# Kernel tuning notes

Measured on AMD Instinct MI355X. Metric: run time of the kernel, lower is better.

The kernel has to match this reference:

```python
import jax, jax.numpy as jnp
import numpy as np
import math

B, N, D, L, H, FF, T = 8, 256, 384, 6, 8, 1536, 4
Dh = D // H  # 48, divisible by 6 for 3D rotary
N_M1 = T + 1 + 2 * N  # learn tokens + state + hand + head
S = 2 * N_M1


def rotary_pe_3d(x, coords):
    # x: [B,H,S,Dh], coords: [B,S,3]. Split head dim into 3 axis chunks,
    # apply standard RoPE per axis using the continuous coordinate as position.
    dh = x.shape[-1]
    d = dh // 3
    half = d // 2
    inv_freq = 1.0 / (10000.0 ** (jnp.arange(half, dtype=x.dtype) / half))
    outs = []
    for a in range(3):
        xa = x[..., a * d:(a + 1) * d]
        ang = coords[..., a][:, None, :, None] * inv_freq  # [B,1,S,half]
        c, s = jnp.cos(ang), jnp.sin(ang)
        x1, x2 = xa[..., :half], xa[..., half:]
        outs.append(jnp.concatenate([x1 * c - x2 * s, x1 * s + x2 * c], axis=-1))
    return jnp.concatenate(outs, axis=-1)


def layernorm(x, g, b):
    m = jnp.mean(x, axis=-1, keepdims=True)
    v = jnp.var(x, axis=-1, keepdims=True)
    return (x - m) * jax.lax.rsqrt(v + 1e-5) * g + b


def transformer_layer(src, coords_src, mask, Wq, bq, Wk, bk, Wv, bv, Wo, bo, W1, b1, W2, b2, g1, be1, g2, be2):
    Bsz, Ss, _ = src.shape
    q = jnp.einsum('bsd,od->bso', src, Wq) + bq
    k = jnp.einsum('bsd,od->bso', src, Wk) + bk
    v = jnp.einsum('bsd,od->bso', src, Wv) + bv
    q = q.reshape(Bsz, Ss, H, Dh).transpose(0, 2, 1, 3)
    k = k.reshape(Bsz, Ss, H, Dh).transpose(0, 2, 1, 3)
    v = v.reshape(Bsz, Ss, H, Dh).transpose(0, 2, 1, 3)
    q = rotary_pe_3d(q, coords_src)
    k = rotary_pe_3d(k, coords_src)
    scores = jnp.einsum('bhqd,bhkd->bhqk', q, k) / math.sqrt(Dh)
    scores = jnp.where(mask[None, None, :, :], -jnp.inf, scores)
    attn = jnp.einsum('bhqk,bhkd->bhqd', jax.nn.softmax(scores, axis=-1), v)
    attn = attn.transpose(0, 2, 1, 3).reshape(Bsz, Ss, D)
    attn = jnp.einsum('bsd,od->bso', attn, Wo) + bo
    src2 = layernorm(src + attn, g1, be1)
    ff = jnp.einsum('bsf,of->bso', jax.nn.gelu(jnp.einsum('bsd,fd->bsf', src2, W1) + b1, approximate=False), W2) + b2
    return layernorm(src2 + ff, g2, be2)


def setup_inputs() -> dict:
    key = jax.random.key(0)
    ks = jax.random.split(key, 32)
    rnd = lambda i, shape, scale=1.0: (jax.random.normal(ks[i], shape, dtype=jnp.float32) * scale)
    inp = {
        'hand_token_t': rnd(0, (B, N, D)),
        'head_token_t': rnd(1, (B, N, D)),
        'hand_token_m1': rnd(2, (B, N, D)),
        'head_token_m1': rnd(3, (B, N, D)),
        'coords_hand_t': rnd(4, (B, N, 3)),
        'coords_head_t': rnd(5, (B, N, 3)),
        'coords_hand_m1': rnd(6, (B, N, 3)),
        'coords_head_m1': rnd(7, (B, N, 3)),
        'state_t': rnd(8, (B, D)),
        'state_m1': rnd(9, (B, D)),
        'trans_head_t': rnd(10, (B, 3)),
        'trans_head_m1': rnd(11, (B, 3)),
        'tokens_m1': rnd(12, (1, T, D), 0.02),
        'tokens_t': rnd(13, (1, T, D), 0.02),
        'Wq': rnd(14, (L, D, D), 0.02), 'bq': jnp.zeros((L, D), jnp.float32),
        'Wk': rnd(15, (L, D, D), 0.02), 'bk': jnp.zeros((L, D), jnp.float32),
        'Wv': rnd(16, (L, D, D), 0.02), 'bv': jnp.zeros((L, D), jnp.float32),
        'Wo': rnd(17, (L, D, D), 0.02), 'bo': jnp.zeros((L, D), jnp.float32),
        'W1': rnd(18, (L, FF, D), 0.02), 'b1': jnp.zeros((L, FF), jnp.float32),
        'W2': rnd(19, (L, D, FF), 0.02), 'b2': jnp.zeros((L, D), jnp.float32),
        'g1': jnp.ones((L, D), jnp.float32), 'be1': jnp.zeros((L, D), jnp.float32),
        'g2': jnp.ones((L, D), jnp.float32), 'be2': jnp.zeros((L, D), jnp.float32),
    }
    return inp


def reference(hand_token_t, head_token_t, hand_token_m1, head_token_m1,
              coords_hand_t, coords_head_t, coords_hand_m1, coords_head_m1,
              state_t, state_m1, trans_head_t, trans_head_m1,
              tokens_m1, tokens_t, Wq, bq, Wk, bk, Wv, bv, Wo, bo,
              W1, b1, W2, b2, g1, be1, g2, be2):
    # Build token sequence: [state_m1, hand_m1, head_m1, learn_m1, state_t, hand_t, head_t, learn_t]
    tok_m1 = jnp.broadcast_to(tokens_m1, (B, T, D))
    tok_t = jnp.broadcast_to(tokens_t, (B, T, D))
    coord_m1 = jnp.broadcast_to(trans_head_m1[:, None, :], (B, T, 3))
    coord_t = jnp.broadcast_to(trans_head_t[:, None, :], (B, T, 3))
    src = jnp.concatenate([
        state_m1[:, None, :], hand_token_m1, head_token_m1, tok_m1,
        state_t[:, None, :], hand_token_t, head_token_t, tok_t], axis=1)
    coords_src = jnp.concatenate([
        trans_head_m1[:, None, :], coords_hand_m1, coords_head_m1, coord_m1,
        trans_head_t[:, None, :], coords_hand_t, coords_head_t, coord_t], axis=1)
    # block-causal mask: m1 block cannot attend to t block
    mask = jnp.zeros((S, S), dtype=bool).at[:N_M1, N_M1:].set(True)
    for i in range(L):
        src = transformer_layer(src, coords_src, mask,
                                Wq[i], bq[i], Wk[i], bk[i], Wv[i], bv[i], Wo[i], bo[i],
                                W1[i], b1[i], W2[i], b2[i], g1[i], be1[i], g2[i], be2[i])
    return src[:, -T:, :]
```

## Files before the change

kernel.cpp:

```cpp
#include <hip/hip_runtime.h>
#include <hip/hip_bf16.h>
#include <math.h>

#define BB 8
#define NN 256
#define DD 384
#define LL 6
#define HH 8
#define FFD 1536
#define TT 4
#define DH 48
#define NM1 517
#define SS 1034
#define SSP 1088
#define MROWS (BB*SS)
#define NQKV 1152
#define QSCALE2 (0.14433756729740643f * 1.4426950408889634f)

typedef unsigned short u16;
typedef unsigned int u32;
typedef short bf8 __attribute__((ext_vector_type(8)));
typedef float f32x4 __attribute__((ext_vector_type(4)));

__device__ __forceinline__ u16 f2bf(float f) {
  __hip_bfloat16 h = __float2bfloat16(f);
  return *reinterpret_cast<u16*>(&h);
}
__device__ __forceinline__ float bf2f(u16 u) {
  __hip_bfloat16 h;
  *reinterpret_cast<u16*>(&h) = u;
  return __bfloat162float(h);
}
__device__ __forceinline__ float max3f(float a, float b, float c) {
  return fmaxf(fmaxf(a, b), c);
}
__device__ __forceinline__ void async16(void* lds, const void* g) {
  __builtin_amdgcn_global_load_lds(
      (const __attribute__((address_space(1))) unsigned int*)g,
      (__attribute__((address_space(3))) unsigned int*)lds, 16, 0, 0);
}

__global__ void build_src(const float* __restrict__ hand_t, const float* __restrict__ head_t,
                          const float* __restrict__ hand_m1, const float* __restrict__ head_m1,
                          const float* __restrict__ state_t, const float* __restrict__ state_m1,
                          const float* __restrict__ tok_m1, const float* __restrict__ tok_t,
                          float* __restrict__ src, u16* __restrict__ srcb) {
  int idx = blockIdx.x * 256 + threadIdx.x;
  if (idx >= BB * SS * DD) return;
  int d = idx % DD;
  int bs = idx / DD;
  int s = bs % SS;
  int b = bs / SS;
  float val;
  if (s == 0)               val = state_m1[b * DD + d];
  else if (s <= NN)         val = hand_m1[((size_t)(b * NN + (s - 1))) * DD + d];
  else if (s <= 2 * NN)     val = head_m1[((size_t)(b * NN + (s - 1 - NN))) * DD + d];
  else if (s <= 2 * NN + TT) val = tok_m1[(s - (2 * NN + 1)) * DD + d];
  else if (s == NM1)        val = state_t[b * DD + d];
  else if (s <= NM1 + NN)   val = hand_t[((size_t)(b * NN + (s - NM1 - 1))) * DD + d];
  else if (s <= NM1 + 2 * NN) val = head_t[((size_t)(b * NN + (s - NM1 - 1 - NN))) * DD + d];
  else                      val = tok_t[(s - (NM1 + 2 * NN + 1)) * DD + d];
  src[idx] = val;
  srcb[idx] = f2bf(val);
}

__global__ void build_coords(const float* __restrict__ c_hand_t, const float* __restrict__ c_head_t,
                             const float* __restrict__ c_hand_m1, const float* __restrict__ c_head_m1,
                             const float* __restrict__ tr_t, const float* __restrict__ tr_m1,
                             float* __restrict__ coords) {
  int idx = blockIdx.x * 256 + threadIdx.x;
  if (idx >= BB * SS * 3) return;
  int a = idx % 3;
  int bs = idx / 3;
  int s = bs % SS;
  int b = bs / SS;
  float val;
  if (s == 0)               val = tr_m1[b * 3 + a];
  else if (s <= NN)         val = c_hand_m1[(b * NN + (s - 1)) * 3 + a];
  else if (s <= 2 * NN)     val = c_head_m1[(b * NN + (s - 1 - NN)) * 3 + a];
  else if (s <= 2 * NN + TT) val = tr_m1[b * 3 + a];
  else if (s == NM1)        val = tr_t[b * 3 + a];
  else if (s <= NM1 + NN)   val = c_hand_t[(b * NN + (s - NM1 - 1)) * 3 + a];
  else if (s <= NM1 + 2 * NN) val = c_head_t[(b * NN + (s - NM1 - 1 - NN)) * 3 + a];
  else                      val = tr_t[b * 3 + a];
  coords[idx] = val;
}

__global__ void build_trig(const float* __restrict__ coords, float2* __restrict__ trig) {
  int idx = blockIdx.x * 256 + threadIdx.x;
  if (idx >= BB * SS * 24) return;
  int i = idx & 7;
  int axis = (idx >> 3) % 3;
  int bs = idx / 24;
  float cv = coords[bs * 3 + axis];
  float inv = expf(-(float)i * 1.1512925464970229f);
  float ang = cv * inv;
  trig[idx] = make_float2(cosf(ang), sinf(ang));
}

__global__ void cvt_bf(const float* __restrict__ in, u16* __restrict__ out, int n4) {
  int idx = blockIdx.x * 256 + threadIdx.x;
  if (idx >= n4) return;
  float4 v = reinterpret_cast<const float4*>(in)[idx];
  short4 o;
  o.x = (short)f2bf(v.x); o.y = (short)f2bf(v.y);
  o.z = (short)f2bf(v.z); o.w = (short)f2bf(v.w);
  reinterpret_cast<short4*>(out)[idx] = o;
}

__global__ void pack_qkv(const float* __restrict__ Wq, const float* __restrict__ Wk,
                         const float* __restrict__ Wv, u16* __restrict__ wqkv) {
  int idx = blockIdx.x * 256 + threadIdx.x;
  const int TOTAL = LL * NQKV * 96;
  if (idx >= TOTAL) return;
  int k4 = idx % 96;
  int n = (idx / 96) % NQKV;
  int l = idx / (96 * NQKV);
  int sel = n / 384, nn = n - sel * 384;
  const float* W = (sel == 0) ? Wq : ((sel == 1) ? Wk : Wv);
  float4 v = *reinterpret_cast<const float4*>(W + ((size_t)l * 384 + nn) * 384 + k4 * 4);
  short4 o;
  o.x = (short)f2bf(v.x); o.y = (short)f2bf(v.y);
  o.z = (short)f2bf(v.z); o.w = (short)f2bf(v.w);
  *reinterpret_cast<short4*>(wqkv + ((size_t)(l * NQKV + n) * 384 + k4 * 4)) = o;
}

__global__ void pack_bqkv(const float* __restrict__ bq, const float* __restrict__ bk,
                          const float* __restrict__ bv, float* __restrict__ bqkv) {
  int idx = blockIdx.x * 256 + threadIdx.x;
  if (idx >= LL * NQKV) return;
  int n = idx % NQKV, l = idx / NQKV;
  int sel = n / 384, nn = n - sel * 384;
  const float* Bp = (sel == 0) ? bq : ((sel == 1) ? bk : bv);
  bqkv[idx] = Bp[l * 384 + nn];
}

__global__ void pad_vt(u16* __restrict__ vt) {
  int idx = blockIdx.x * 256 + threadIdx.x;
  const int PADW = SSP - SS;
  if (idx >= 64 * DH * PADW) return;
  int c = idx % PADW;
  int rd = idx / PADW;
  vt[(size_t)rd * SSP + SS + c] = 0;
}

__global__ void pad_qk(u16* __restrict__ qh, u16* __restrict__ kh) {
  int idx = blockIdx.x * 256 + threadIdx.x;
  if (idx >= 64 * SS * 16) return;
  int c = idx & 15;
  int row = idx >> 4;
  qh[(size_t)row * 64 + 48 + c] = 0;
  kh[(size_t)row * 64 + 48 + c] = 0;
}

template <int EPI, int OUT, int Nc, int Kc>
__global__ __launch_bounds__(512) void gemm_as(
    const u16* __restrict__ Ab, const u16* __restrict__ Wb,
    const float* __restrict__ bias, const float2* __restrict__ trig,
    const float* __restrict__ Rf,
    float* __restrict__ Cf, u16* __restrict__ Cb,
    u16* __restrict__ Ck, u16* __restrict__ Cv) {
  constexpr int BUFSZ = 24576;
  constexpr int M = MROWS;
  constexpr int nxt = Nc >> 6;
  __shared__ __align__(16) char sm[2 * BUFSZ];
  const int tid = threadIdx.x;

  const int gL = blockIdx.x;
  const int x8 = gL & 7, jj = gL >> 3;
  const int jjm = jj / nxt;
  const int cnt = (x8 == 0) ? 9 : 8;
  if (jjm >= cnt) return;
  const int mt_ = ((x8 == 0) ? 0 : 9 + (x8 - 1) * 8) + jjm;
  const int bm = mt_ << 7, bn = (jj % nxt) << 6;

  const int lid = tid & 63, w = tid >> 6;
  const int wm = w >> 1, wn = w & 1;
  const int l15 = lid & 15, lg = lid >> 4;
  const int lr = lid >> 3, lu = lid & 7;
  const int swz = lu ^ lr;
  f32x4 acc[2][2] = {};

  auto stage = [&](int bsel, int k0) {
    char* base = sm + bsel * BUFSZ;
#pragma unroll
    for (int q = 0; q < 2; ++q) {
      int row = w * 16 + q * 8 + lr;
      int grow = bm + row; if (grow >= M) grow = M - 1;
      async16(base + w * 2048 + q * 1024, Ab + (size_t)grow * Kc + k0 + (swz << 3));
    }
    async16(base + 16384 + w * 1024, Wb + (size_t)(bn + w * 8 + lr) * Kc + k0 + (swz << 3));
  };

  stage(0, 0);
  int bs = 0;

#pragma unroll
  for (int k0 = 0; k0 < Kc; k0 += 64) {
    if (k0 + 64 < Kc) {
      stage(bs ^ 1, k0 + 64);
      asm volatile("s_waitcnt vmcnt(3)" ::: "memory");
    } else {
      asm volatile("s_waitcnt vmcnt(0)" ::: "memory");
    }
    __builtin_amdgcn_s_barrier();
    const char* base = sm + bs * BUFSZ;
    bf8 a[2][2], bfr[2][2];
#pragma unroll
    for (int kf = 0; kf < 2; ++kf) {
#pragma unroll
      for (int mt = 0; mt < 2; ++mt) {
        int row = wm * 32 + mt * 16 + l15;
        int off = ((row << 7) + (kf << 6) + (lg << 4)) ^ ((row & 7) << 4);
        a[kf][mt] = *reinterpret_cast<const bf8*>(base + off);
      }
#pragma unroll
      for (int nt = 0; nt < 2; ++nt) {
        int row = wn * 32 + nt * 16 + l15;
        int off = 16384 + (((row << 7) + (kf << 6) + (lg << 4)) ^ ((row & 7) << 4));
        bfr[kf][nt] = *reinterpret_cast<const bf8*>(base + off);
      }
    }
#pragma unroll
    for (int kf = 0; kf < 2; ++kf)
#pragma unroll
      for (int mt = 0; mt < 2; ++mt)
#pragma unroll
        for (int nt = 0; nt < 2; ++nt)
          acc[mt][nt] = __builtin_amdgcn_mfma_f32_16x16x32_bf16(a[kf][mt], bfr[kf][nt], acc[mt][nt], 0, 0, 0);
    asm volatile("s_waitcnt lgkmcnt(0)" ::: "memory");
    __builtin_amdgcn_s_barrier();
    bs ^= 1;
  }

  if constexpr (OUT != 2) {
#pragma unroll
    for (int nt = 0; nt < 2; ++nt) {
      const int n = bn + wn * 32 + nt * 16 + l15;
      const float bsv = bias[n];
#pragma unroll
      for (int mt = 0; mt < 2; ++mt) {
        const int m0 = bm + wm * 32 + mt * 16 + lg * 4;
#pragma unroll
        for (int r = 0; r < 4; ++r) {
          int m = m0 + r;
          if (m >= M) continue;
          float v = acc[mt][nt][r] + bsv;
          if (EPI == 1) v = 0.5f * v * (1.0f + erff(v * 0.70710678118654752f));
          if (OUT == 0) Cf[(size_t)m * Nc + n] = v + Rf[(size_t)m * Nc + n];
          else          Cb[(size_t)m * Nc + n] = f2bf(v);
        }
      }
    }
  } else {
    float* tile = (float*)sm;
#pragma unroll
    for (int nt = 0; nt < 2; ++nt) {
      const int nl = wn * 32 + nt * 16 + l15;
      const float bsv = bias[bn + nl];
#pragma unroll
      for (int mt = 0; mt < 2; ++mt) {
#pragma unroll
        for (int r = 0; r < 4; ++r) {
          int ml = wm * 32 + mt * 16 + lg * 4 + r;
          tile[ml * 65 + nl] = acc[mt][nt][r] + bsv;
        }
      }
    }
    __syncthreads();
    const int bnm = bn % 384;
    const int sel = bn / 384;
    if (sel < 2) {
      u16* Cqk = (sel == 0) ? Cb : Ck;
      const int d = lid;
      const int nn_ = bnm + d;
      const int hdiv = nn_ / 48, hrem = nn_ - hdiv * 48;
      const int axis = hrem >> 4, ii = hrem & 7;
      const bool hi = (hrem & 8) != 0;
      for (int si = 0; si < 16; ++si) {
        int row = w * 16 + si;
        int m = bm + row;
        if (m >= M) break;
        int bI = m / SS, s = m - bI * SS;
        float v = tile[row * 65 + d];
        float p = tile[row * 65 + (d ^ 8)];
        float2 t = trig[(size_t)(bI * SS + s) * 24 + axis * 8 + ii];
        float outv = hi ? (p * t.y + v * t.x) : (v * t.x - p * t.y);
        if (sel == 0) outv *= QSCALE2;
        Cqk[((size_t)(bI * HH + hdiv) * SS + s) * 64 + hrem] = f2bf(outv);
      }
    } else {
      const int srow = tid & 127, dq = tid >> 7;
      const int m = bm + srow;
      if (m < M) {
        int bI = m / SS, s = m - bI * SS;
        for (int di = 0; di < 16; ++di) {
          int d = dq * 16 + di;
          int nn_ = bnm + d;
          int hdiv = nn_ / 48, hrem = nn_ - hdiv * 48;
          Cv[((size_t)(bI * HH + hdiv) * DH + hrem) * SSP + s] = f2bf(tile[srow * 65 + d]);
        }
      }
    }
  }
}

__global__ __launch_bounds__(512) void attn_mfma(const u16* __restrict__ qh,
                                                 const u16* __restrict__ kh,
                                                 const u16* __restrict__ vt,
                                                 u16* __restrict__ outb) {
  __shared__ __align__(16) char sm[32768];
  const int tid = threadIdx.x;
  const int lid = tid & 63, w = tid >> 6;
  const int l15 = lid & 15, lg = lid >> 4;
  const int lr = lid >> 3, lu = lid & 7;
  const int swz8 = (lu ^ lr) << 3;

  const int f = blockIdx.x;
  const int low = f & 7, j = f >> 3;
  const int gi = j / 9, qp = j - gi * 9;
  const int g = gi * 8 + low;
  const int h = g & 7, b = g >> 3;
  const int qblk = (qp < 5) ? (4 + qp) : (qp - 5);
  const int bh = b * HH + h;
  const int q0w = qblk * 128 + w * 16;
  const u16* kbase = kh + (size_t)bh * SS * 64;
  const u16* vbase = vt + (size_t)bh * DH * SSP;

  bf8 qf[2];
  {
    int row = q0w + l15; if (row >= SS) row = SS - 1;
    const u16* qp_ = qh + ((size_t)bh * SS + row) * 64;
    qf[0] = *reinterpret_cast<const bf8*>(qp_ + lg * 8);
    qf[1] = *reinterpret_cast<const bf8*>(qp_ + 32 + lg * 8);
  }
  const int qrow = q0w + l15;

  float m_q = -1e30f, l_q = 0.f;
  f32x4 accO[3] = {};

  const int nch = (qblk < 4) ? 9 : 17;

  auto stage = [&](int bsel, int c) {
    const int j0 = c * 64;
    char* kb = sm + bsel * 16384;
    char* vb = kb + 8192;
    {
      int s = w * 8 + lr;
      int jt_ = s >> 4, lgs = (s >> 2) & 3, rr = s & 3;
      int p = ((jt_ >> 1) << 5) + (lgs << 3) + ((jt_ & 1) << 2) + rr;
      int jrow = j0 + p; if (jrow >= SS) jrow = SS - 1;
      async16(kb + w * 1024, kbase + (size_t)jrow * 64 + swz8);
    }
    {
      int vrow = w * 8 + lr; if (vrow >= DH) vrow = DH - 1;
      async16(vb + w * 1024, vbase + (size_t)vrow * SSP + j0 + swz8);
    }
  };

  stage(0, 0);
  __syncthreads();
  int bsel = 0;

  for (int c = 0; c < nch; ++c) {
    if (c + 1 < nch) {
      stage(bsel ^ 1, c + 1);
      asm volatile("s_waitcnt vmcnt(2)" ::: "memory");
    } else {
      asm volatile("s_waitcnt vmcnt(0)" ::: "memory");
    }
    __builtin_amdgcn_s_barrier();
    const int j0 = c * 64;
    const char* kb = sm + bsel * 16384;
    const char* vb = kb + 8192;

    f32x4 sv[4];
    __builtin_amdgcn_s_setprio(1);
#pragma unroll
    for (int jt = 0; jt < 4; ++jt) {
      int row = jt * 16 + l15;
      int off0 = ((row << 7) + (lg << 4)) ^ ((row & 7) << 4);
      int off1 = ((row << 7) + 64 + (lg << 4)) ^ ((row & 7) << 4);
      bf8 kb0 = *reinterpret_cast<const bf8*>(kb + off0);
      bf8 kb1 = *reinterpret_cast<const bf8*>(kb + off1);
      f32x4 z = {};
      z = __builtin_amdgcn_mfma_f32_16x16x32_bf16(kb0, qf[0], z, 0, 0, 0);
      z = __builtin_amdgcn_mfma_f32_16x16x32_bf16(kb1, qf[1], z, 0, 0, 0);
      sv[jt] = z;
    }
    __builtin_amdgcn_s_setprio(0);

    const bool domask = (c == 16) | ((q0w < NM1) & (c >= 8));
    if (domask) {
#pragma unroll
      for (int jt = 0; jt < 4; ++jt)
#pragma unroll
        for (int r = 0; r < 4; ++r) {
          int kabs = j0 + ((jt >> 1) << 5) + (lg << 3) + ((jt & 1) << 2) + r;
          if (kabs >= SS || (qrow < NM1 && kabs >= NM1)) sv[jt][r] = -1e30f;
        }
    }

    float mx = max3f(sv[0][0], sv[0][1], sv[0][2]);
    mx = max3f(mx, sv[0][3], sv[1][0]);
    mx = max3f(mx, sv[1][1], sv[1][2]);
    mx = max3f(mx, sv[1][3], sv[2][0]);
    mx = max3f(mx, sv[2][1], sv[2][2]);
    mx = max3f(mx, sv[2][3], sv[3][0]);
    mx = max3f(mx, sv[3][1], sv[3][2]);
    mx = fmaxf(mx, sv[3][3]);
    mx = fmaxf(mx, __shfl_xor(mx, 16));
    mx = fmaxf(mx, __shfl_xor(mx, 32));

    const bool skip = __all(mx <= m_q);
    const float mn = skip ? m_q : fmaxf(m_q, mx);

    float pv[4][4];
    float ps = 0.f;
#pragma unroll
    for (int jt = 0; jt < 4; ++jt)
#pragma unroll
      for (int r = 0; r < 4; ++r) {
        float p = __builtin_amdgcn_exp2f(sv[jt][r] - mn);
        pv[jt][r] = p;
        ps += p;
      }
    ps += __shfl_xor(ps, 16);
    ps += __shfl_xor(ps, 32);

    if (!skip) {
      float alpha = __builtin_amdgcn_exp2f(m_q - mn);
      l_q = l_q * alpha + ps;
      m_q = mn;
      const int lg4 = lg * 4;
      float a0 = __shfl(alpha, lg4);
      float a1 = __shfl(alpha, lg4 + 1);
      float a2 = __shfl(alpha, lg4 + 2);
      float a3 = __shfl(alpha, lg4 + 3);
#pragma unroll
      for (int dt = 0; dt < 3; ++dt) {
        accO[dt][0] *= a0; accO[dt][1] *= a1;
        accO[dt][2] *= a2; accO[dt][3] *= a3;
      }
    } else {
      l_q += ps;
    }

    bf8 pa[2];
#pragma unroll
    for (int jc = 0; jc < 2; ++jc) {
      u32 w0 = (u32)f2bf(pv[jc * 2][0])     | ((u32)f2bf(pv[jc * 2][1]) << 16);
      u32 w1 = (u32)f2bf(pv[jc * 2][2])     | ((u32)f2bf(pv[jc * 2][3]) << 16);
      u32 w2 = (u32)f2bf(pv[jc * 2 + 1][0]) | ((u32)f2bf(pv[jc * 2 + 1][1]) << 16);
      u32 w3 = (u32)f2bf(pv[jc * 2 + 1][2]) | ((u32)f2bf(pv[jc * 2 + 1][3]) << 16);
      uint4 t = make_uint4(w0, w1, w2, w3);
      pa[jc] = *reinterpret_cast<bf8*>(&t);
    }

    __builtin_amdgcn_s_setprio(1);
#pragma unroll
    for (int dt = 0; dt < 3; ++dt) {
      int row = dt * 16 + l15;
#pragma unroll
      for (int jc = 0; jc < 2; ++jc) {
        int off = ((row << 7) + (jc << 6) + (lg << 4)) ^ ((row & 7) << 4);
        bf8 vb8 = *reinterpret_cast<const bf8*>(vb + off);
        accO[dt] = __builtin_amdgcn_mfma_f32_16x16x32_bf16(pa[jc], vb8, accO[dt], 0, 0, 0);
      }
    }
    __builtin_amdgcn_s_setprio(0);
    asm volatile("s_waitcnt lgkmcnt(0)" ::: "memory");
    __builtin_amdgcn_s_barrier();
    bsel ^= 1;
  }

  float linv = 1.0f / l_q;
  const int lg4 = lg * 4;
  float il[4];
#pragma unroll
  for (int r = 0; r < 4; ++r) il[r] = __shfl(linv, lg4 + r);
#pragma unroll
  for (int r = 0; r < 4; ++r) {
    int q = q0w + lg4 + r;
    if (q >= SS) continue;
#pragma unroll
    for (int dt = 0; dt < 3; ++dt) {
      int d = dt * 16 + l15;
      outb[((size_t)(b * SS + q)) * DD + h * DH + d] = f2bf(accO[dt][r] * il[r]);
    }
  }
}

__global__ __launch_bounds__(512) void add_ln(const float* __restrict__ a,
                                              const float* __restrict__ g,
                                              const float* __restrict__ be,
                                              float* __restrict__ out,
                                              u16* __restrict__ outb) {
  const int w = threadIdx.x >> 6, lane = threadIdx.x & 63;
  const int row = blockIdx.x * 8 + w;
  const size_t base = (size_t)row * DD;
  float x[6];
#pragma unroll
  for (int jj = 0; jj < 6; ++jj) x[jj] = a[base + lane + 64 * jj];
  float s = x[0] + x[1] + x[2] + x[3] + x[4] + x[5];
#pragma unroll
  for (int off = 32; off; off >>= 1) s += __shfl_xor(s, off);
  float mean = s * (1.0f / 384.0f);
  float dv[6], vs = 0.f;
#pragma unroll
  for (int jj = 0; jj < 6; ++jj) { dv[jj] = x[jj] - mean; vs += dv[jj] * dv[jj]; }
#pragma unroll
  for (int off = 32; off; off >>= 1) vs += __shfl_xor(vs, off);
  float rs = rsqrtf(vs * (1.0f / 384.0f) + 1e-5f);
#pragma unroll
  for (int jj = 0; jj < 6; ++jj) {
    int c = lane + 64 * jj;
    float o = dv[jj] * rs * g[c] + be[c];
    out[base + c] = o;
    outb[base + c] = f2bf(o);
  }
}

__global__ void copy_out(const float* __restrict__ src, float* __restrict__ out) {
  int idx = blockIdx.x * 256 + threadIdx.x;
  if (idx >= BB * TT * DD) return;
  int d = idx % DD;
  int bt = idx / DD;
  int t = bt % TT;
  int b = bt / TT;
  out[idx] = src[((size_t)b * SS + (SS - TT) + t) * DD + d];
}

extern "C" void kernel_launch(void* const* d_in, const int* in_sizes, int n_in,
                              void* d_out, int out_size, void* d_ws, size_t ws_size,
                              hipStream_t stream) {
  const float* hand_t    = (const float*)d_in[0];
  const float* head_t    = (const float*)d_in[1];
  const float* hand_m1   = (const float*)d_in[2];
  const float* head_m1   = (const float*)d_in[3];
  const float* c_hand_t  = (const float*)d_in[4];
  const float* c_head_t  = (const float*)d_in[5];
  const float* c_hand_m1 = (const float*)d_in[6];
  const float* c_head_m1 = (const float*)d_in[7];
  const float* state_t   = (const float*)d_in[8];
  const float* state_m1  = (const float*)d_in[9];
  const float* tr_t      = (const float*)d_in[10];
  const float* tr_m1     = (const float*)d_in[11];
  const float* tok_m1    = (const float*)d_in[12];
  const float* tok_t     = (const float*)d_in[13];
  const float* Wq = (const float*)d_in[14];
  const float* bq = (const float*)d_in[15];
  const float* Wk = (const float*)d_in[16];
  const float* bk = (const float*)d_in[17];
  const float* Wv = (const float*)d_in[18];
  const float* bv = (const float*)d_in[19];
  const float* Wo = (const float*)d_in[20];
  const float* bo = (const float*)d_in[21];
  const float* W1 = (const float*)d_in[22];
  const float* b1 = (const float*)d_in[23];
  const float* W2 = (const float*)d_in[24];
  const float* b2 = (const float*)d_in[25];
  const float* g1 = (const float*)d_in[26];
  const float* be1 = (const float*)d_in[27];
  const float* g2 = (const float*)d_in[28];
  const float* be2 = (const float*)d_in[29];

  const size_t SRC_N = (size_t)BB * SS * DD;
  float* src    = (float*)d_ws;
  float* src2   = src + SRC_N;
  float* bufB   = src2 + SRC_N;
  float* coords = bufB + SRC_N;
  float* bqkv   = coords + (size_t)BB * SS * 3;
  float2* trig  = (float2*)(bqkv + (size_t)LL * NQKV);
  u16* srcb  = (u16*)(trig + (size_t)BB * SS * 24);
  u16* src2b = srcb + SRC_N;
  u16* attnb = src2b + SRC_N;
  u16* qh  = attnb + SRC_N;
  const size_t QH_N = (size_t)BB * HH * SS * 64;
  u16* khb = qh + QH_N;
  u16* vtb = khb + QH_N;
  u16* hbf = vtb + (size_t)64 * DH * SSP;
  u16* wqkv_b = hbf + (size_t)MROWS * FFD;
  const size_t WD = (size_t)LL * DD * DD;
  const size_t WF = (size_t)LL * FFD * DD;
  u16* wo_bf = wqkv_b + (size_t)LL * NQKV * 384;
  u16* w1_bf = wo_bf + WD;
  u16* w2_bf = w1_bf + WF;

  dim3 blk(256);
  dim3 blk512(512);

  build_src<<<(BB * SS * DD + 255) / 256, blk, 0, stream>>>(
      hand_t, head_t, hand_m1, head_m1, state_t, state_m1, tok_m1, tok_t, src, srcb);
  build_coords<<<(BB * SS * 3 + 255) / 256, blk, 0, stream>>>(
      c_hand_t, c_head_t, c_hand_m1, c_head_m1, tr_t, tr_m1, coords);
  build_trig<<<(BB * SS * 24 + 255) / 256, blk, 0, stream>>>(coords, trig);
  pack_qkv<<<(LL * NQKV * 96 + 255) / 256, blk, 0, stream>>>(Wq, Wk, Wv, wqkv_b);
  pack_bqkv<<<(LL * NQKV + 255) / 256, blk, 0, stream>>>(bq, bk, bv, bqkv);
  cvt_bf<<<(int)(WD / 4 + 255) / 256, blk, 0, stream>>>(Wo, wo_bf, (int)(WD / 4));
  cvt_bf<<<(int)(WF / 4 + 255) / 256, blk, 0, stream>>>(W1, w1_bf, (int)(WF / 4));
  cvt_bf<<<(int)(WF / 4 + 255) / 256, blk, 0, stream>>>(W2, w2_bf, (int)(WF / 4));
  pad_vt<<<(64 * DH * (SSP - SS) + 255) / 256, blk, 0, stream>>>(vtb);
  pad_qk<<<(64 * SS * 16 + 255) / 256, blk, 0, stream>>>(qh, khb);

  dim3 gqkv(18 * 72);
  dim3 gwo(6 * 72);
  dim3 gf1(24 * 72);
  dim3 gf2(6 * 72);
  dim3 gattn(9 * 8 * 8);

  for (int l = 0; l < LL; ++l) {
    const u16* Wqkv_l = wqkv_b + (size_t)l * NQKV * 384;
    const u16* Wo_l = wo_bf + (size_t)l * DD * DD;
    const u16* W1_l = w1_bf + (size_t)l * FFD * DD;
    const u16* W2_l = w2_bf + (size_t)l * DD * FFD;

    gemm_as<0, 2, NQKV, DD><<<gqkv, blk512, 0, stream>>>(
        srcb, Wqkv_l, bqkv + l * NQKV, trig, nullptr, nullptr, qh, khb, vtb);
    attn_mfma<<<gattn, blk512, 0, stream>>>(qh, khb, vtb, attnb);
    gemm_as<0, 0, DD, DD><<<gwo, blk512, 0, stream>>>(
        attnb, Wo_l, bo + l * DD, nullptr, src, bufB, nullptr, nullptr, nullptr);
    add_ln<<<MROWS / 8, blk512, 0, stream>>>(bufB, g1 + l * DD, be1 + l * DD, src2, src2b);
    gemm_as<1, 1, FFD, DD><<<gf1, blk512, 0, stream>>>(
        src2b, W1_l, b1 + l * FFD, nullptr, nullptr, nullptr, hbf, nullptr, nullptr);
    gemm_as<0, 0, DD, FFD><<<gf2, blk512, 0, stream>>>(
        hbf, W2_l, b2 + l * DD, nullptr, src2, bufB, nullptr, nullptr, nullptr);
    add_ln<<<MROWS / 8, blk512, 0, stream>>>(bufB, g2 + l * DD, be2 + l * DD, src, srcb);
  }
  copy_out<<<(BB * TT * DD + 255) / 256, blk, 0, stream>>>(src, (float*)d_out);
}
```

Baseline: 873.9 us.

## Fold LayerNorm into adjacent GEMMs via row stats and weight-scaled gamma

Removes the standalone add_ln kernels. Row sums and sums of squares are now accumulated atomically in the residual GEMM epilogues, and a tiny stats_fin kernel turns them into mean and rstd. The LN gamma is folded into the next GEMM's weights, and beta plus the mean correction go in as per-column constants (G and C), so the QKV and W1 GEMMs consume the un-normalized bf16 residual and normalize in the epilogue. This cuts memory passes per layer, at the cost of numerics: variance is computed as E[x^2]-mu^2, the un-normalized input is rounded to bf16, and float atomics make the order nondeterministic.

```diff
diff --git a/kernel.cpp b/kernel.cpp
--- a/kernel.cpp
+++ b/kernel.cpp
@@ -109,7 +109,8 @@
 }
 
 __global__ void pack_qkv(const float* __restrict__ Wq, const float* __restrict__ Wk,
-                         const float* __restrict__ Wv, u16* __restrict__ wqkv) {
+                         const float* __restrict__ Wv, const float* __restrict__ g2,
+                         u16* __restrict__ wqkv) {
   int idx = blockIdx.x * 256 + threadIdx.x;
   const int TOTAL = LL * NQKV * 96;
   if (idx >= TOTAL) return;
@@ -119,10 +120,28 @@
   int sel = n / 384, nn = n - sel * 384;
   const float* W = (sel == 0) ? Wq : ((sel == 1) ? Wk : Wv);
   float4 v = *reinterpret_cast<const float4*>(W + ((size_t)l * 384 + nn) * 384 + k4 * 4);
+  float4 gg = make_float4(1.f, 1.f, 1.f, 1.f);
+  if (l > 0) gg = *reinterpret_cast<const float4*>(g2 + (size_t)(l - 1) * 384 + k4 * 4);
   short4 o;
-  o.x = (short)f2bf(v.x); o.y = (short)f2bf(v.y);
-  o.z = (short)f2bf(v.z); o.w = (short)f2bf(v.w);
+  o.x = (short)f2bf(v.x * gg.x); o.y = (short)f2bf(v.y * gg.y);
+  o.z = (short)f2bf(v.z * gg.z); o.w = (short)f2bf(v.w * gg.w);
   *reinterpret_cast<short4*>(wqkv + ((size_t)(l * NQKV + n) * 384 + k4 * 4)) = o;
+}
+
+__global__ void pack_w1(const float* __restrict__ W1, const float* __restrict__ g1,
+                        u16* __restrict__ w1f) {
+  int idx = blockIdx.x * 256 + threadIdx.x;
+  const int TOTAL = LL * FFD * 96;
+  if (idx >= TOTAL) return;
+  int k4 = idx % 96;
+  int n = (idx / 96) % FFD;
+  int l = idx / (96 * FFD);
+  float4 v = *reinterpret_cast<const float4*>(W1 + ((size_t)l * FFD + n) * 384 + k4 * 4);
+  float4 gg = *reinterpret_cast<const float4*>(g1 + (size_t)l * 384 + k4 * 4);
+  short4 o;
+  o.x = (short)f2bf(v.x * gg.x); o.y = (short)f2bf(v.y * gg.y);
+  o.z = (short)f2bf(v.z * gg.z); o.w = (short)f2bf(v.w * gg.w);
+  *reinterpret_cast<short4*>(w1f + ((size_t)(l * FFD + n) * 384 + k4 * 4)) = o;
 }
 
 __global__ void pack_bqkv(const float* __restrict__ bq, const float* __restrict__ bk,
@@ -135,6 +154,57 @@
   bqkv[idx] = Bp[l * 384 + nn];
 }
 
+__global__ void qkv_consts(const u16* __restrict__ wqkvf,
+                           const float* __restrict__ Wq, const float* __restrict__ Wk,
+                           const float* __restrict__ Wv, const float* __restrict__ bqkv,
+                           const float* __restrict__ be2,
+                           float* __restrict__ G, float* __restrict__ C) {
+  int gid = blockIdx.x * 4 + (threadIdx.x >> 6);
+  int lane = threadIdx.x & 63;
+  if (gid >= LL * NQKV) return;
+  int l = gid / NQKV, n = gid % NQKV;
+  int sel = n / 384, nn = n - sel * 384;
+  const float* W = (sel == 0) ? Wq : ((sel == 1) ? Wk : Wv);
+  float s = 0.f, c = 0.f;
+  for (int k = lane; k < 384; k += 64) {
+    s += bf2f(wqkvf[(size_t)gid * 384 + k]);
+    float bek = (l == 0) ? 0.f : be2[(l - 1) * 384 + k];
+    c += bek * W[((size_t)l * 384 + nn) * 384 + k];
+  }
+#pragma unroll
+  for (int off = 32; off; off >>= 1) { s += __shfl_xor(s, off); c += __shfl_xor(c, off); }
+  if (lane == 0) { G[gid] = s; C[gid] = c + bqkv[gid]; }
+}
+
+__global__ void w1_consts(const u16* __restrict__ w1f, const float* __restrict__ W1,
+                          const float* __restrict__ b1, const float* __restrict__ be1,
+                          float* __restrict__ G, float* __restrict__ C) {
+  int gid = blockIdx.x * 4 + (threadIdx.x >> 6);
+  int lane = threadIdx.x & 63;
+  if (gid >= LL * FFD) return;
+  int l = gid / FFD, n = gid % FFD;
+  float s = 0.f, c = 0.f;
+  for (int k = lane; k < 384; k += 64) {
+    s += bf2f(w1f[(size_t)gid * 384 + k]);
+    c += be1[l * 384 + k] * W1[((size_t)l * FFD + n) * 384 + k];
+  }
+#pragma unroll
+  for (int off = 32; off; off >>= 1) { s += __shfl_xor(s, off); c += __shfl_xor(c, off); }
+  if (lane == 0) { G[gid] = s; C[gid] = c + b1[gid]; }
+}
+
+__global__ void stats_fin(float* __restrict__ acc, float* __restrict__ fin) {
+  int m = blockIdx.x * 256 + threadIdx.x;
+  if (m >= MROWS) return;
+  float s = acc[2 * m], ss = acc[2 * m + 1];
+  float mu = s * (1.0f / 384.0f);
+  float var = ss * (1.0f / 384.0f) - mu * mu;
+  fin[2 * m] = mu;
+  fin[2 * m + 1] = rsqrtf(var + 1e-5f);
+  acc[2 * m] = 0.f;
+  acc[2 * m + 1] = 0.f;
+}
+
 __global__ void pad_vt(u16* __restrict__ vt) {
   int idx = blockIdx.x * 256 + threadIdx.x;
   const int PADW = SSP - SS;
@@ -153,13 +223,19 @@
   kh[(size_t)row * 64 + 48 + c] = 0;
 }
 
-template <int EPI, int OUT, int Nc, int Kc>
+template <int EPI, int OUT, int Nc, int Kc, int FOLD, int RES>
 __global__ __launch_bounds__(512) void gemm_as(
     const u16* __restrict__ Ab, const u16* __restrict__ Wb,
-    const float* __restrict__ bias, const float2* __restrict__ trig,
+    const float* __restrict__ bias,
+    const float* __restrict__ Gv, const float* __restrict__ Cvv,
+    const float* __restrict__ stA,
+    const float2* __restrict__ trig,
     const float* __restrict__ Rf,
+    const float* __restrict__ RfL, const float* __restrict__ stR,
+    const float* __restrict__ gR, const float* __restrict__ beR,
     float* __restrict__ Cf, u16* __restrict__ Cb,
-    u16* __restrict__ Ck, u16* __restrict__ Cv) {
+    u16* __restrict__ Ck, u16* __restrict__ Cvt,
+    float* __restrict__ sAcc) {
   constexpr int BUFSZ = 24576;
   constexpr int M = MROWS;
   constexpr int nxt = Nc >> 6;
@@ -233,11 +309,10 @@
     bs ^= 1;
   }
 
-  if constexpr (OUT != 2) {
+  if constexpr (OUT == 1) {
 #pragma unroll
     for (int nt = 0; nt < 2; ++nt) {
       const int n = bn + wn * 32 + nt * 16 + l15;
-      const float bsv = bias[n];
 #pragma unroll
       for (int mt = 0; mt < 2; ++mt) {
         const int m0 = bm + wm * 32 + mt * 16 + lg * 4;
@@ -245,25 +320,89 @@
         for (int r = 0; r < 4; ++r) {
           int m = m0 + r;
           if (m >= M) continue;
-          float v = acc[mt][nt][r] + bsv;
+          float v;
+          if constexpr (FOLD) {
+            float mu = stA[2 * m], rsv = stA[2 * m + 1];
+            v = rsv * acc[mt][nt][r] + Cvv[n] - mu * rsv * Gv[n];
+          } else {
+            v = acc[mt][nt][r] + bias[n];
+          }
           if (EPI == 1) v = 0.5f * v * (1.0f + erff(v * 0.70710678118654752f));
-          if (OUT == 0) Cf[(size_t)m * Nc + n] = v + Rf[(size_t)m * Nc + n];
-          else          Cb[(size_t)m * Nc + n] = f2bf(v);
+          Cb[(size_t)m * Nc + n] = f2bf(v);
         }
       }
     }
+  } else if constexpr (OUT == 0) {
+    float vv[2][2][4];
+#pragma unroll
+    for (int nt = 0; nt < 2; ++nt) {
+      const int n = bn + wn * 32 + nt * 16 + l15;
+#pragma unroll
+      for (int mt = 0; mt < 2; ++mt) {
+        const int m0 = bm + wm * 32 + mt * 16 + lg * 4;
+#pragma unroll
+        for (int r = 0; r < 4; ++r) {
+          int m = m0 + r;
+          int mc = (m < M) ? m : (M - 1);
+          float v;
+          if constexpr (FOLD) {
+            float mu = stA[2 * mc], rsv = stA[2 * mc + 1];
+            v = rsv * acc[mt][nt][r] + Cvv[n] - mu * rsv * Gv[n];
+          } else {
+            v = acc[mt][nt][r] + bias[n];
+          }
+          if (EPI == 1) v = 0.5f * v * (1.0f + erff(v * 0.70710678118654752f));
+          if constexpr (RES == 1) {
+            v += Rf[(size_t)mc * Nc + n];
+          } else if constexpr (RES == 2) {
+            float x = RfL[(size_t)mc * Nc + n];
+            float muR = stR[2 * mc], rsR = stR[2 * mc + 1];
+            v += (x - muR) * rsR * gR[n] + beR[n];
+          }
+          vv[mt][nt][r] = v;
+          if (m < M) {
+            Cf[(size_t)m * Nc + n] = v;
+            Cb[(size_t)m * Nc + n] = f2bf(v);
+          }
+        }
+      }
+    }
+#pragma unroll
+    for (int mt = 0; mt < 2; ++mt)
+#pragma unroll
+      for (int r = 0; r < 4; ++r) {
+        int m = bm + wm * 32 + mt * 16 + lg * 4 + r;
+        float s = vv[mt][0][r] + vv[mt][1][r];
+        float ss = vv[mt][0][r] * vv[mt][0][r] + vv[mt][1][r] * vv[mt][1][r];
+        s += __shfl_xor(s, 1);  ss += __shfl_xor(ss, 1);
+        s += __shfl_xor(s, 2);  ss += __shfl_xor(ss, 2);
+        s += __shfl_xor(s, 4);  ss += __shfl_xor(ss, 4);
+        s += __shfl_xor(s, 8);  ss += __shfl_xor(ss, 8);
+        if (l15 == 0 && m < M) {
+          atomicAdd(&sAcc[2 * m], s);
+          atomicAdd(&sAcc[2 * m + 1], ss);
+        }
+      }
   } else {
     float* tile = (float*)sm;
 #pragma unroll
     for (int nt = 0; nt < 2; ++nt) {
       const int nl = wn * 32 + nt * 16 + l15;
-      const float bsv = bias[bn + nl];
+      const int n = bn + nl;
 #pragma unroll
       for (int mt = 0; mt < 2; ++mt) {
 #pragma unroll
         for (int r = 0; r < 4; ++r) {
           int ml = wm * 32 + mt * 16 + lg * 4 + r;
-          tile[ml * 65 + nl] = acc[mt][nt][r] + bsv;
+          float v;
+          if constexpr (FOLD) {
+            int mc = bm + ml; if (mc >= M) mc = M - 1;
+            float mu = stA[2 * mc], rsv = stA[2 * mc + 1];
+            v = rsv * acc[mt][nt][r] + Cvv[n] - mu * rsv * Gv[n];
+          } else {
+            v = acc[mt][nt][r] + bias[n];
+          }
+          tile[ml * 65 + nl] = v;
         }
       }
     }
@@ -298,7 +437,7 @@
           int d = dq * 16 + di;
           int nn_ = bnm + d;
           int hdiv = nn_ / 48, hrem = nn_ - hdiv * 48;
-          Cv[((size_t)(bI * HH + hdiv) * DH + hrem) * SSP + s] = f2bf(tile[srow * 65 + d]);
+          Cvt[((size_t)(bI * HH + hdiv) * DH + hrem) * SSP + s] = f2bf(tile[srow * 65 + d]);
         }
       }
     }
@@ -491,44 +630,18 @@
   }
 }
 
-__global__ __launch_bounds__(512) void add_ln(const float* __restrict__ a,
-                                              const float* __restrict__ g,
-                                              const float* __restrict__ be,
-                                              float* __restrict__ out,
-                                              u16* __restrict__ outb) {
-  const int w = threadIdx.x >> 6, lane = threadIdx.x & 63;
-  const int row = blockIdx.x * 8 + w;
-  const size_t base = (size_t)row * DD;
-  float x[6];
-#pragma unroll
-  for (int jj = 0; jj < 6; ++jj) x[jj] = a[base + lane + 64 * jj];
-  float s = x[0] + x[1] + x[2] + x[3] + x[4] + x[5];
-#pragma unroll
-  for (int off = 32; off; off >>= 1) s += __shfl_xor(s, off);
-  float mean = s * (1.0f / 384.0f);
-  float dv[6], vs = 0.f;
-#pragma unroll
-  for (int jj = 0; jj < 6; ++jj) { dv[jj] = x[jj] - mean; vs += dv[jj] * dv[jj]; }
-#pragma unroll
-  for (int off = 32; off; off >>= 1) vs += __shfl_xor(vs, off);
-  float rs = rsqrtf(vs * (1.0f / 384.0f) + 1e-5f);
-#pragma unroll
-  for (int jj = 0; jj < 6; ++jj) {
-    int c = lane + 64 * jj;
-    float o = dv[jj] * rs * g[c] + be[c];
-    out[base + c] = o;
-    outb[base + c] = f2bf(o);
-  }
-}
-
-__global__ void copy_out(const float* __restrict__ src, float* __restrict__ out) {
+__global__ void copy_out(const float* __restrict__ rf2, const float* __restrict__ st,
+                         const float* __restrict__ g, const float* __restrict__ be,
+                         float* __restrict__ out) {
   int idx = blockIdx.x * 256 + threadIdx.x;
   if (idx >= BB * TT * DD) return;
   int d = idx % DD;
   int bt = idx / DD;
   int t = bt % TT;
   int b = bt / TT;
-  out[idx] = src[((size_t)b * SS + (SS - TT) + t) * DD + d];
+  int m = b * SS + (SS - TT) + t;
+  float mu = st[2 * m], rs = st[2 * m + 1];
+  out[idx] = (rf2[(size_t)m * DD + d] - mu) * rs * g[d] + be[d];
 }
 
 extern "C" void kernel_launch(void* const* d_in, const int* in_sizes, int n_in,
@@ -567,14 +680,23 @@
 
   const size_t SRC_N = (size_t)BB * SS * DD;
   float* src    = (float*)d_ws;
-  float* src2   = src + SRC_N;
-  float* bufB   = src2 + SRC_N;
-  float* coords = bufB + SRC_N;
+  float* rf1    = src + SRC_N;
+  float* rf2    = rf1 + SRC_N;
+  float* coords = rf2 + SRC_N;
   float* bqkv   = coords + (size_t)BB * SS * 3;
-  float2* trig  = (float2*)(bqkv + (size_t)LL * NQKV);
+  float* sAcc1  = bqkv + (size_t)LL * NQKV;
+  float* sAcc2  = sAcc1 + 2 * MROWS;
+  float* stF1   = sAcc2 + 2 * MROWS;
+  float* stF2   = stF1 + 2 * MROWS;
+  float* Gq     = stF2 + 2 * MROWS;
+  float* Cq     = Gq + (size_t)LL * NQKV;
+  float* G1     = Cq + (size_t)LL * NQKV;
+  float* C1     = G1 + (size_t)LL * FFD;
+  float2* trig  = (float2*)(C1 + (size_t)LL * FFD);
   u16* srcb  = (u16*)(trig + (size_t)BB * SS * 24);
-  u16* src2b = srcb + SRC_N;
-  u16* attnb = src2b + SRC_N;
+  u16* rb1   = srcb + SRC_N;
+  u16* rb2   = rb1 + SRC_N;
+  u16* attnb = rb2 + SRC_N;
   u16* qh  = attnb + SRC_N;
   const size_t QH_N = (size_t)BB * HH * SS * 64;
   u16* khb = qh + QH_N;
@@ -590,16 +712,20 @@
   dim3 blk(256);
   dim3 blk512(512);
 
+  hipMemsetAsync(sAcc1, 0, 4 * MROWS * sizeof(float), stream);
+
   build_src<<<(BB * SS * DD + 255) / 256, blk, 0, stream>>>(
       hand_t, head_t, hand_m1, head_m1, state_t, state_m1, tok_m1, tok_t, src, srcb);
   build_coords<<<(BB * SS * 3 + 255) / 256, blk, 0, stream>>>(
       c_hand_t, c_head_t, c_hand_m1, c_head_m1, tr_t, tr_m1, coords);
   build_trig<<<(BB * SS * 24 + 255) / 256, blk, 0, stream>>>(coords, trig);
-  pack_qkv<<<(LL * NQKV * 96 + 255) / 256, blk, 0, stream>>>(Wq, Wk, Wv, wqkv_b);
+  pack_qkv<<<(LL * NQKV * 96 + 255) / 256, blk, 0, stream>>>(Wq, Wk, Wv, g2, wqkv_b);
   pack_bqkv<<<(LL * NQKV + 255) / 256, blk, 0, stream>>>(bq, bk, bv, bqkv);
+  pack_w1<<<(LL * FFD * 96 + 255) / 256, blk, 0, stream>>>(W1, g1, w1_bf);
   cvt_bf<<<(int)(WD / 4 + 255) / 256, blk, 0, stream>>>(Wo, wo_bf, (int)(WD / 4));
-  cvt_bf<<<(int)(WF / 4 + 255) / 256, blk, 0, stream>>>(W1, w1_bf, (int)(WF / 4));
   cvt_bf<<<(int)(WF / 4 + 255) / 256, blk, 0, stream>>>(W2, w2_bf, (int)(WF / 4));
+  qkv_consts<<<(LL * NQKV + 3) / 4, blk, 0, stream>>>(wqkv_b, Wq, Wk, Wv, bqkv, be2, Gq, Cq);
+  w1_consts<<<(LL * FFD + 3) / 4, blk, 0, stream>>>(w1_bf, W1, b1, be1, G1, C1);
   pad_vt<<<(64 * DH * (SSP - SS) + 255) / 256, blk, 0, stream>>>(vtb);
   pad_qk<<<(64 * SS * 16 + 255) / 256, blk, 0, stream>>>(qh, khb);
 
@@ -608,6 +734,7 @@
   dim3 gf1(24 * 72);
   dim3 gf2(6 * 72);
   dim3 gattn(9 * 8 * 8);
+  dim3 gsf((MROWS + 255) / 256);
 
   for (int l = 0; l < LL; ++l) {
     const u16* Wqkv_l = wqkv_b + (size_t)l * NQKV * 384;
@@ -615,17 +742,40 @@
     const u16* W1_l = w1_bf + (size_t)l * FFD * DD;
     const u16* W2_l = w2_bf + (size_t)l * DD * FFD;
 
-    gemm_as<0, 2, NQKV, DD><<<gqkv, blk512, 0, stream>>>(
-        srcb, Wqkv_l, bqkv + l * NQKV, trig, nullptr, nullptr, qh, khb, vtb);
+    if (l == 0) {
+      gemm_as<0, 2, NQKV, DD, 0, 0><<<gqkv, blk512, 0, stream>>>(
+          srcb, Wqkv_l, bqkv, nullptr, nullptr, nullptr, trig,
+          nullptr, nullptr, nullptr, nullptr, nullptr,
+          nullptr, qh, khb, vtb, nullptr);
+    } else {
+      gemm_as<0, 2, NQKV, DD, 1, 0><<<gqkv, blk512, 0, stream>>>(
+          rb2, Wqkv_l, nullptr, Gq + (size_t)l * NQKV, Cq + (size_t)l * NQKV, stF2, trig,
+          nullptr, nullptr, nullptr, nullptr, nullptr,
+          nullptr, qh, khb, vtb, nullptr);
+    }
     attn_mfma<<<gattn, blk512, 0, stream>>>(qh, khb, vtb, attnb);
-    gemm_as<0, 0, DD, DD><<<gwo, blk512, 0, stream>>>(
-        attnb, Wo_l, bo + l * DD, nullptr, src, bufB, nullptr, nullptr, nullptr);
-    add_ln<<<MROWS / 8, blk512, 0, stream>>>(bufB, g1 + l * DD, be1 + l * DD, src2, src2b);
-    gemm_as<1, 1, FFD, DD><<<gf1, blk512, 0, stream>>>(
-        src2b, W1_l, b1 + l * FFD, nullptr, nullptr, nullptr, hbf, nullptr, nullptr);
-    gemm_as<0, 0, DD, FFD><<<gf2, blk512, 0, stream>>>(
-        hbf, W2_l, b2 + l * DD, nullptr, src2, bufB, nullptr, nullptr, nullptr);
-    add_ln<<<MROWS / 8, blk512, 0, stream>>>(bufB, g2 + l * DD, be2 + l * DD, src, srcb);
+    if (l == 0) {
+      gemm_as<0, 0, DD, DD, 0, 1><<<gwo, blk512, 0, stream>>>(
+          attnb, Wo_l, bo + l * DD, nullptr, nullptr, nullptr, nullptr,
+          src, nullptr, nullptr, nullptr, nullptr,
+          rf1, rb1, nullptr, nullptr, sAcc1);
+    } else {
+      gemm_as<0, 0, DD, DD, 0, 2><<<gwo, blk512, 0, stream>>>(
+          attnb, Wo_l, bo + l * DD, nullptr, nullptr, nullptr, nullptr,
+          nullptr, rf2, stF2, g2 + (l - 1) * DD, be2 + (l - 1) * DD,
+          rf1, rb1, nullptr, nullptr, sAcc1);
+    }
+    stats_fin<<<gsf, blk, 0, stream>>>(sAcc1, stF1);
+    gemm_as<1, 1, FFD, DD, 1, 0><<<gf1, blk512, 0, stream>>>(
+        rb1, W1_l, nullptr, G1 + (size_t)l * FFD, C1 + (size_t)l * FFD, stF1, nullptr,
+        nullptr, nullptr, nullptr, nullptr, nullptr,
+        nullptr, hbf, nullptr, nullptr, nullptr);
+    gemm_as<0, 0, DD, FFD, 0, 2><<<gf2, blk512, 0, stream>>>(
+        hbf, W2_l, b2 + l * DD, nullptr, nullptr, nullptr, nullptr,
+        nullptr, rf1, stF1, g1 + l * DD, be1 + l * DD,
+        rf2, rb2, nullptr, nullptr, sAcc2);
+    stats_fin<<<gsf, blk, 0, stream>>>(sAcc2, stF2);
   }
-  copy_out<<<(BB * TT * DD + 255) / 256, blk, 0, stream>>>(src, (float*)d_out);
-}
+  copy_out<<<(BB * TT * DD + 255) / 256, blk, 0, stream>>>(
+      rf2, stF2, g2 + 5 * DD, be2 + 5 * DD, (float*)d_out);
+}
```

Result: slower. 1.004 ms (+14.8%).
